# Kernel tuning notes

Measured on AMD Instinct MI355X. Metric: run time of the kernel, lower is better.

The kernel has to match this reference:

```python
import math
import jax, jax.numpy as jnp
import numpy as np

NTYPE, C, H, E = 3, 256, 8, 32  # n_embd=256, n_head=8, edge_dim=32
A1 = 16  # aux_x1 feature dim (aux_x2 dim = E - A1)


def setup_inputs() -> dict:
    key = jax.random.key(0)
    ks = jax.random.split(key, 16)
    B, T1, T2 = 8, 128, 256
    s = 0.02
    return {
        "x1": jax.random.normal(ks[0], (B, T1, C), jnp.float32),
        "x2": jax.random.normal(ks[1], (B, T2, C), jnp.float32),
        "aux_x1": jax.random.normal(ks[2], (B, T1, A1), jnp.float32),
        "aux_x2": jax.random.normal(ks[3], (B, T2, E - A1), jnp.float32),
        "masks": jax.random.randint(ks[4], (NTYPE, B, T1, T2), 0, 2, jnp.int32),
        # per-type linear params, stored (in, out) so y = x @ W + b
        "Wq": jax.random.normal(ks[5], (NTYPE, C, C), jnp.float32) * s,
        "bq": jnp.zeros((NTYPE, C), jnp.float32),
        "Wk": jax.random.normal(ks[6], (NTYPE, C + E, C), jnp.float32) * s,
        "bk": jnp.zeros((NTYPE, C), jnp.float32),
        "Wv": jax.random.normal(ks[7], (NTYPE, C + E, C), jnp.float32) * s,
        "bv": jnp.zeros((NTYPE, C), jnp.float32),
        "Wp": jax.random.normal(ks[8], (NTYPE, C, C), jnp.float32) * s,
        "bp": jnp.zeros((NTYPE, C), jnp.float32),
    }


def _aux_attn(x1, x2, aux_x1, aux_x2, mask, Wq, bq, Wk, bk, Wv, bv, Wp, bp):
    """One AuxCrossAttention type. mask: (B,T1,T2) int."""
    B, T1, _ = x1.shape
    T2 = x2.shape[1]
    hd = C // H
    scale = 1.0 / math.sqrt(hd)

    q = x1 @ Wq + bq  # (B,T1,C)
    # k/v over aug_x2 = [x2 | aux_x1 | aux_x2]; split the linear instead of
    # materializing the (B,T1,T2,C+E) concat (same math by linearity).
    Wk_x, Wk_a1, Wk_a2 = Wk[:C], Wk[C:C + A1], Wk[C + A1:]
    Wv_x, Wv_a1, Wv_a2 = Wv[:C], Wv[C:C + A1], Wv[C + A1:]
    k = (x2 @ Wk_x + aux_x2 @ Wk_a2 + bk)[:, None] + (aux_x1 @ Wk_a1)[:, :, None]  # (B,T1,T2,C)
    v = (x2 @ Wv_x + aux_x2 @ Wv_a2 + bv)[:, None] + (aux_x1 @ Wv_a1)[:, :, None]  # (B,T1,T2,C)

    qh = q.reshape(B, T1, H, hd)
    kh = k.reshape(B, T1, T2, H, hd)
    vh = v.reshape(B, T1, T2, H, hd)

    att = jnp.einsum("bthd,btshd->bhts", qh, kh) * scale  # (B,H,T1,T2)
    valid = (mask != 0)[:, None]  # (B,1,T1,T2)
    att = jnp.where(valid, att, -jnp.inf)
    all_masked = (mask == 0).all(-1)  # (B,T1)
    att = jnp.where(all_masked[:, None, :, None], 0.0, att)
    f = jnp.finfo(att.dtype)
    att = jnp.nan_to_num(att, nan=0.0, posinf=f.max, neginf=f.min)
    att = jax.nn.softmax(att, axis=-1)

    y = jnp.einsum("bhts,btshd->bthd", att, vh).reshape(B, T1, C)
    return y @ Wp + bp


def reference(x1, x2, aux_x1, aux_x2, masks, Wq, bq, Wk, bk, Wv, bv, Wp, bp):
    resid = jnp.zeros_like(x1)
    for i in range(NTYPE):
        resid = resid + _aux_attn(x1, x2, aux_x1, aux_x2, masks[i],
                                  Wq[i], bq[i], Wk[i], bk[i], Wv[i], bv[i], Wp[i], bp[i])
    return resid
```

## Files before the change

kernel.cpp:

```cpp
#include <hip/hip_runtime.h>
#include <hip/hip_bf16.h>

#define NC 256
#define HD 32
#define KE 288

typedef __attribute__((ext_vector_type(8))) short short8;
typedef __attribute__((ext_vector_type(4))) short short4v;
typedef __attribute__((ext_vector_type(4))) float f32x4;

__device__ __forceinline__ unsigned short f2bf(float f) {
    union { float f; unsigned u; } v; v.f = f;
    unsigned r = v.u + 0x7fffu + ((v.u >> 16) & 1u);
    return (unsigned short)(r >> 16);
}

__global__ __launch_bounds__(256) void fused_qkv(
    const float* __restrict__ x1, const float* __restrict__ x2,
    const float* __restrict__ ax1, const float* __restrict__ ax2,
    const float* __restrict__ Wq, const float* __restrict__ bq,
    const float* __restrict__ Wk, const float* __restrict__ bk,
    const float* __restrict__ Wv, const float* __restrict__ bv,
    float* __restrict__ q, float* __restrict__ kb, float* __restrict__ vb,
    float* __restrict__ va)
{
    __shared__ short As[4 * 128 * 8];
    __shared__ short Bs[4 * 128 * 8];

    const int bx = blockIdx.x;
    const float *Aab, *Aaux, *W, *bias;
    float* outp;
    int m0, n0, nfull, auxrow;
    if (bx < 48) {
        const int i = bx >> 4, tile = bx & 15;
        m0 = (tile >> 1) * 128; n0 = (tile & 1) * 128;
        Aab = x1; Aaux = nullptr;
        W = Wq + i * NC * NC; bias = bq + i * NC;
        outp = q + (size_t)i * 1024 * NC; nfull = 8; auxrow = -1;
    } else if (bx < 240) {
        const int idx = bx - 48, i2 = idx >> 5, tile = idx & 31;
        const int i = i2 % 3, kv = i2 / 3;
        m0 = (tile >> 1) * 128; n0 = (tile & 1) * 128;
        Aab = x2; Aaux = ax2;
        W = (kv ? Wv : Wk) + i * KE * NC; bias = (kv ? bv : bk) + i * NC;
        outp = (kv ? vb : kb) + (size_t)i * 2048 * NC; nfull = 8; auxrow = 272;
    } else {
        const int idx = bx - 240, i = idx >> 4, tile = idx & 15;
        m0 = (tile >> 1) * 128; n0 = (tile & 1) * 128;
        Aab = nullptr; Aaux = ax1;
        W = Wv + i * KE * NC; bias = nullptr;
        outp = va + (size_t)i * 1024 * NC; nfull = 0; auxrow = 256;
    }

    const int tid = threadIdx.x;
    const int m8 = tid >> 3, kq = tid & 7;
    const int kk = tid >> 3, nq = tid & 7;
    const int wave = tid >> 6, lane = tid & 63;
    const int wy = wave >> 1, wx = wave & 1;
    const int qd = lane >> 4, ml = lane & 15;

    f32x4 acc[4][4];
#pragma unroll
    for (int a = 0; a < 4; ++a)
#pragma unroll
        for (int b = 0; b < 4; ++b) acc[a][b] = {0.f, 0.f, 0.f, 0.f};

    const int nsteps = nfull + (auxrow >= 0 ? 1 : 0);
    for (int step = 0; step < nsteps; ++step) {
        const bool aux = (step == nfull);
        {
            const float* Ap; int lda, kval;
            if (!aux) { Ap = Aab + (size_t)m0 * NC + step * 32; lda = NC; kval = 32; }
            else      { Ap = Aaux + (size_t)m0 * 16;            lda = 16; kval = 16; }
#pragma unroll
            for (int rep = 0; rep < 4; ++rep) {
                const int m = m8 + rep * 32;
                float4 a4 = {0.f, 0.f, 0.f, 0.f};
                if (kq * 4 < kval) a4 = *(const float4*)(Ap + (size_t)m * lda + kq * 4);
                short4v s;
                s.x = (short)f2bf(a4.x); s.y = (short)f2bf(a4.y);
                s.z = (short)f2bf(a4.z); s.w = (short)f2bf(a4.w);
                *(short4v*)&As[(((kq >> 1) * 128) + m) * 8 + (kq & 1) * 4] = s;
            }
        }
        {
            const int krow0 = aux ? auxrow : step * 32;
            const int kval  = aux ? 16 : 32;
#pragma unroll
            for (int rep = 0; rep < 4; ++rep) {
                const int n = nq * 4 + rep * 32;
                float4 b4 = {0.f, 0.f, 0.f, 0.f};
                if (kk < kval) b4 = *(const float4*)(W + (size_t)(krow0 + kk) * NC + n0 + n);
                const int base = (kk >> 3) * 128;
                const int kw = kk & 7;
                Bs[(base + n + 0) * 8 + kw] = (short)f2bf(b4.x);
                Bs[(base + n + 1) * 8 + kw] = (short)f2bf(b4.y);
                Bs[(base + n + 2) * 8 + kw] = (short)f2bf(b4.z);
                Bs[(base + n + 3) * 8 + kw] = (short)f2bf(b4.w);
            }
        }
        __syncthreads();
        short8 af[4], bfr[4];
#pragma unroll
        for (int mt = 0; mt < 4; ++mt)
            af[mt] = *(const short8*)&As[((qd * 128) + wy * 64 + mt * 16 + ml) * 8];
#pragma unroll
        for (int nt = 0; nt < 4; ++nt)
            bfr[nt] = *(const short8*)&Bs[((qd * 128) + wx * 64 + nt * 16 + ml) * 8];
#pragma unroll
        for (int mt = 0; mt < 4; ++mt)
#pragma unroll
            for (int nt = 0; nt < 4; ++nt)
                acc[mt][nt] = __builtin_amdgcn_mfma_f32_16x16x32_bf16(
                    af[mt], bfr[nt], acc[mt][nt], 0, 0, 0);
        __syncthreads();
    }
#pragma unroll
    for (int nt = 0; nt < 4; ++nt) {
        const int col = n0 + wx * 64 + nt * 16 + ml;
        const float bsv = bias ? bias[col] : 0.f;
#pragma unroll
        for (int mt = 0; mt < 4; ++mt) {
            const int row0 = m0 + wy * 64 + mt * 16 + qd * 4;
#pragma unroll
            for (int r = 0; r < 4; ++r)
                outp[(size_t)(row0 + r) * NC + col] = acc[mt][nt][r] + bsv;
        }
    }
}

__global__ __launch_bounds__(256) void attn_mfma(
    const float* __restrict__ q, const float* __restrict__ kb,
    const float* __restrict__ vb, const float* __restrict__ va,
    const int* __restrict__ masks, float* __restrict__ y)
{
    const int bx = blockIdx.x;
    const int tc = bx & 1, h = (bx >> 1) & 7, b = (bx >> 4) & 7, i = bx >> 7;
    const size_t bb = (size_t)i * 8 + b;

    __shared__ short Ks[4 * 256 * 8];
    __shared__ short Vt[32 * 32 * 8];
    __shared__ short Ps[4][32 * 16 * 8];

    const int tid = threadIdx.x;
    const int wave = tid >> 6, lane = tid & 63;
    const int ml = lane & 15, qd = lane >> 4;

    {
        const float* kp = kb + (bb * 256 + tid) * NC + h * HD;
#pragma unroll
        for (int j = 0; j < 8; ++j) {
            float4 v = *(const float4*)(kp + j * 4);
            short4v s;
            s.x = (short)f2bf(v.x); s.y = (short)f2bf(v.y);
            s.z = (short)f2bf(v.z); s.w = (short)f2bf(v.w);
            *(short4v*)&Ks[(((j >> 1) * 256) + tid) * 8 + (j & 1) * 4] = s;
        }
    }
    {
        const int d = tid & 31, sg8 = tid >> 5;
#pragma unroll
        for (int it = 0; it < 4; ++it) {
            const int s0 = it * 64 + sg8 * 8;
            const float* vp = vb + (bb * 256 + s0) * NC + h * HD + d;
            short8 s8;
#pragma unroll
            for (int u = 0; u < 8; ++u) s8[u] = (short)f2bf(vp[u * NC]);
            *(short8*)&Vt[((s0 >> 3) * 32 + d) * 8] = s8;
        }
    }
    __syncthreads();

    const float qscale = 0.17677669529663687f * 1.4426950408889634f;
    short8 af;
    {
        const int t = tc * 64 + wave * 16 + ml;
        const float* qp = q + (bb * 128 + t) * NC + h * HD + qd * 8;
        float4 q0 = *(const float4*)qp;
        float4 q1 = *(const float4*)(qp + 4);
        af[0] = (short)f2bf(q0.x * qscale); af[1] = (short)f2bf(q0.y * qscale);
        af[2] = (short)f2bf(q0.z * qscale); af[3] = (short)f2bf(q0.w * qscale);
        af[4] = (short)f2bf(q1.x * qscale); af[5] = (short)f2bf(q1.y * qscale);
        af[6] = (short)f2bf(q1.z * qscale); af[7] = (short)f2bf(q1.w * qscale);
    }

    f32x4 sacc[16];
#pragma unroll
    for (int nt = 0; nt < 16; ++nt) sacc[nt] = {0.f, 0.f, 0.f, 0.f};
#pragma unroll
    for (int nt = 0; nt < 16; ++nt) {
        short8 bf = *(const short8*)&Ks[(qd * 256 + nt * 16 + ml) * 8];
        sacc[nt] = __builtin_amdgcn_mfma_f32_16x16x32_bf16(af, bf, sacc[nt], 0, 0, 0);
    }

    const int tb = tc * 64 + wave * 16 + qd * 4;
    const int* mp = masks + bb * 128 * 256 + (size_t)tb * 256 + ml;
    f32x4 rs = {0.f, 0.f, 0.f, 0.f};
#pragma unroll
    for (int nt = 0; nt < 16; ++nt) {
#pragma unroll
        for (int r = 0; r < 4; ++r) {
            const int mk = mp[r * 256 + nt * 16];
            float e = mk ? __builtin_amdgcn_exp2f(sacc[nt][r]) : 0.f;
            sacc[nt][r] = e;
            rs[r] += e;
        }
    }
#pragma unroll
    for (int off = 1; off <= 8; off <<= 1) {
#pragma unroll
        for (int r = 0; r < 4; ++r) rs[r] += __shfl_xor(rs[r], off);
    }
    f32x4 pinv, pfill;
#pragma unroll
    for (int r = 0; r < 4; ++r) {
        const bool z = (rs[r] == 0.f);
        pinv[r]  = z ? 0.f : 1.f / rs[r];
        pfill[r] = z ? (1.f / 256.f) : 0.f;
    }

    short* Pw = &Ps[wave][0];
#pragma unroll
    for (int nt = 0; nt < 16; ++nt) {
        const int sgrp = 2 * nt + (ml >> 3);
        const int pos = ml & 7;
#pragma unroll
        for (int r = 0; r < 4; ++r) {
            const float p = sacc[nt][r] * pinv[r] + pfill[r];
            Pw[(sgrp * 16 + qd * 4 + r) * 8 + pos] = (short)f2bf(p);
        }
    }

    f32x4 oacc[2];
    oacc[0] = {0.f, 0.f, 0.f, 0.f};
    oacc[1] = {0.f, 0.f, 0.f, 0.f};
#pragma unroll
    for (int ks = 0; ks < 8; ++ks) {
        short8 pa = *(const short8*)&Pw[((ks * 4 + qd) * 16 + ml) * 8];
#pragma unroll
        for (int n2 = 0; n2 < 2; ++n2) {
            short8 vf = *(const short8*)&Vt[((ks * 4 + qd) * 32 + n2 * 16 + ml) * 8];
            oacc[n2] = __builtin_amdgcn_mfma_f32_16x16x32_bf16(pa, vf, oacc[n2], 0, 0, 0);
        }
    }

#pragma unroll
    for (int n2 = 0; n2 < 2; ++n2) {
        const int d = n2 * 16 + ml;
#pragma unroll
        for (int r = 0; r < 4; ++r) {
            const size_t idx = (bb * 128 + tb + r) * NC + h * HD + d;
            y[idx] = oacc[n2][r] + va[idx];
        }
    }
}

__global__ __launch_bounds__(256) void proj_mfma(
    const float* __restrict__ y, const float* __restrict__ Wp,
    const float* __restrict__ bp, float* __restrict__ out)
{
    __shared__ short As[4 * 64 * 8];
    __shared__ short Bs[4 * 64 * 8];

    const int bx = blockIdx.x;
    const int m0 = (bx >> 2) * 64, n0 = (bx & 3) * 64;
    const int tid = threadIdx.x;
    const int m8 = tid >> 3, kq = tid & 7;
    const int kk = tid >> 3, nq = tid & 7;
    const int wave = tid >> 6, lane = tid & 63;
    const int wy = wave >> 1, wx = wave & 1;
    const int qd = lane >> 4, ml = lane & 15;

    f32x4 acc[2][2];
#pragma unroll
    for (int a = 0; a < 2; ++a)
#pragma unroll
        for (int b = 0; b < 2; ++b) acc[a][b] = {0.f, 0.f, 0.f, 0.f};

    for (int i = 0; i < 3; ++i) {
        const float* A = y + (size_t)i * 1024 * NC;
        const float* W = Wp + (size_t)i * NC * NC;
        for (int step = 0; step < 8; ++step) {
#pragma unroll
            for (int rep = 0; rep < 2; ++rep) {
                const int m = m8 + rep * 32;
                float4 a4 = *(const float4*)(A + (size_t)(m0 + m) * NC + step * 32 + kq * 4);
                short4v s;
                s.x = (short)f2bf(a4.x); s.y = (short)f2bf(a4.y);
                s.z = (short)f2bf(a4.z); s.w = (short)f2bf(a4.w);
                *(short4v*)&As[(((kq >> 1) * 64) + m) * 8 + (kq & 1) * 4] = s;
            }
#pragma unroll
            for (int rep = 0; rep < 2; ++rep) {
                const int n = nq * 4 + rep * 32;
                float4 b4 = *(const float4*)(W + (size_t)(step * 32 + kk) * NC + n0 + n);
                const int base = (kk >> 3) * 64;
                const int kw = kk & 7;
                Bs[(base + n + 0) * 8 + kw] = (short)f2bf(b4.x);
                Bs[(base + n + 1) * 8 + kw] = (short)f2bf(b4.y);
                Bs[(base + n + 2) * 8 + kw] = (short)f2bf(b4.z);
                Bs[(base + n + 3) * 8 + kw] = (short)f2bf(b4.w);
            }
            __syncthreads();
            short8 af[2], bfr[2];
#pragma unroll
            for (int mt = 0; mt < 2; ++mt)
                af[mt] = *(const short8*)&As[((qd * 64) + wy * 32 + mt * 16 + ml) * 8];
#pragma unroll
            for (int nt = 0; nt < 2; ++nt)
                bfr[nt] = *(const short8*)&Bs[((qd * 64) + wx * 32 + nt * 16 + ml) * 8];
#pragma unroll
            for (int mt = 0; mt < 2; ++mt)
#pragma unroll
                for (int nt = 0; nt < 2; ++nt)
                    acc[mt][nt] = __builtin_amdgcn_mfma_f32_16x16x32_bf16(
                        af[mt], bfr[nt], acc[mt][nt], 0, 0, 0);
            __syncthreads();
        }
    }
#pragma unroll
    for (int nt = 0; nt < 2; ++nt) {
        const int col = n0 + wx * 32 + nt * 16 + ml;
        const float b3 = bp[col] + bp[NC + col] + bp[2 * NC + col];
#pragma unroll
        for (int mt = 0; mt < 2; ++mt) {
            const int row0 = m0 + wy * 32 + mt * 16 + qd * 4;
#pragma unroll
            for (int r = 0; r < 4; ++r)
                out[(size_t)(row0 + r) * NC + col] = acc[mt][nt][r] + b3;
        }
    }
}

extern "C" void kernel_launch(void* const* d_in, const int* in_sizes, int n_in,
                              void* d_out, int out_size, void* d_ws, size_t ws_size,
                              hipStream_t stream)
{
    const float* x1  = (const float*)d_in[0];
    const float* x2  = (const float*)d_in[1];
    const float* ax1 = (const float*)d_in[2];
    const float* ax2 = (const float*)d_in[3];
    const int*   mk  = (const int*)d_in[4];
    const float* Wq  = (const float*)d_in[5];
    const float* bq  = (const float*)d_in[6];
    const float* Wk  = (const float*)d_in[7];
    const float* bk  = (const float*)d_in[8];
    const float* Wv  = (const float*)d_in[9];
    const float* bv  = (const float*)d_in[10];
    const float* Wp  = (const float*)d_in[11];
    const float* bp  = (const float*)d_in[12];

    float* ws = (float*)d_ws;
    float* q  = ws;
    float* kb = q  + 3 * 1024 * 256;
    float* vb = kb + 3 * 2048 * 256;
    float* va = vb + 3 * 2048 * 256;
    float* y  = va + 3 * 1024 * 256;

    fused_qkv<<<dim3(288), 256, 0, stream>>>(x1, x2, ax1, ax2, Wq, bq, Wk, bk,
                                             Wv, bv, q, kb, vb, va);
    attn_mfma<<<dim3(384), 256, 0, stream>>>(q, kb, vb, va, mk, y);
    proj_mfma<<<dim3(64), 256, 0, stream>>>(y, Wp, bp, (float*)d_out);
}
```

Baseline: 135.6 us.

## Pre-convert inputs and weights to bf16 MFMA layouts, pack masks into bitmasks

Adds a prep kernel that converts activations and weights to bf16 in K-contiguous (transposed) layouts and packs the int32 masks into per-row bitmasks. The GEMM and attention kernels then read MFMA fragments straight from global memory with no LDS staging or barriers. Intermediates q, k, transposed v and y are stored in bf16, which halves their traffic. This costs an extra kernel launch and a weight conversion on every call, and the fragment loads from global memory may be less coalesced than the old staged path.

```diff
diff --git a/kernel.cpp b/kernel.cpp
--- a/kernel.cpp
+++ b/kernel.cpp
@@ -3,7 +3,6 @@
 
 #define NC 256
 #define HD 32
-#define KE 288
 
 typedef __attribute__((ext_vector_type(8))) short short8;
 typedef __attribute__((ext_vector_type(4))) short short4v;
@@ -14,47 +13,157 @@
     unsigned r = v.u + 0x7fffu + ((v.u >> 16) & 1u);
     return (unsigned short)(r >> 16);
 }
-
-__global__ __launch_bounds__(256) void fused_qkv(
+__device__ __forceinline__ short8 cvt8(float4 a, float4 b) {
+    short8 s;
+    s[0] = (short)f2bf(a.x); s[1] = (short)f2bf(a.y);
+    s[2] = (short)f2bf(a.z); s[3] = (short)f2bf(a.w);
+    s[4] = (short)f2bf(b.x); s[5] = (short)f2bf(b.y);
+    s[6] = (short)f2bf(b.z); s[7] = (short)f2bf(b.w);
+    return s;
+}
+
+__global__ __launch_bounds__(256) void prep(
     const float* __restrict__ x1, const float* __restrict__ x2,
     const float* __restrict__ ax1, const float* __restrict__ ax2,
-    const float* __restrict__ Wq, const float* __restrict__ bq,
-    const float* __restrict__ Wk, const float* __restrict__ bk,
-    const float* __restrict__ Wv, const float* __restrict__ bv,
-    float* __restrict__ q, float* __restrict__ kb, float* __restrict__ vb,
-    float* __restrict__ va)
+    const float* __restrict__ Wq, const float* __restrict__ Wk,
+    const float* __restrict__ Wv, const float* __restrict__ Wp,
+    const int* __restrict__ masks,
+    short* __restrict__ x1b, short* __restrict__ A2, short* __restrict__ ax1p,
+    short* __restrict__ WqT, short* __restrict__ WkT, short* __restrict__ WvT,
+    short* __restrict__ WvA1T, short* __restrict__ WpT,
+    unsigned int* __restrict__ mb)
 {
-    __shared__ short As[4 * 128 * 8];
-    __shared__ short Bs[4 * 128 * 8];
-
+    const int bx = blockIdx.x, tid = threadIdx.x;
+    const short8 zero8 = {0, 0, 0, 0, 0, 0, 0, 0};
+
+    if (bx < 64) {
+        const size_t base = ((size_t)bx * 256 + tid) * 16;
+        const float* p = x1 + base;
+        float4 a = *(const float4*)p,       b = *(const float4*)(p + 4);
+        float4 c = *(const float4*)(p + 8), d = *(const float4*)(p + 12);
+        *(short8*)&x1b[base]     = cvt8(a, b);
+        *(short8*)&x1b[base + 8] = cvt8(c, d);
+    } else if (bx < 96) {
+        const int r0 = (bx - 64) * 64;
+        for (int rr = 0; rr < 64; ++rr) {
+            const int row = r0 + rr;
+            A2[row * 288 + tid] = (short)f2bf(x2[(size_t)row * 256 + tid]);
+            if (tid < 16)
+                A2[row * 288 + 256 + tid] = (short)f2bf(ax2[row * 16 + tid]);
+            else if (tid < 32)
+                A2[row * 288 + 256 + tid] = 0;
+        }
+    } else if (bx < 100) {
+        const int row = (bx - 96) * 256 + tid;
+        const float* p = ax1 + (size_t)row * 16;
+        float4 a = *(const float4*)p,       b = *(const float4*)(p + 4);
+        float4 c = *(const float4*)(p + 8), d = *(const float4*)(p + 12);
+        short* o = ax1p + (size_t)row * 32;
+        *(short8*)o        = cvt8(a, b);
+        *(short8*)(o + 8)  = cvt8(c, d);
+        *(short8*)(o + 16) = zero8;
+        *(short8*)(o + 24) = zero8;
+    } else if (bx < 112) {
+        const int idx = bx - 100, i = idx >> 2, o0 = (idx & 3) * 8;
+        const float* W = Wq + (size_t)i * 256 * 256;
+        short* O = WqT + (size_t)i * 256 * 256;
+        for (int o = o0; o < o0 + 8; ++o) {
+            short8 s;
+#pragma unroll
+            for (int j = 0; j < 8; ++j) s[j] = (short)f2bf(W[(size_t)(o * 8 + j) * 256 + tid]);
+            *(short8*)&O[(size_t)tid * 256 + o * 8] = s;
+        }
+    } else if (bx < 136) {
+        const int idx = bx - 112, kv = idx / 12, sub = idx % 12;
+        const int i = sub >> 2, o0 = (sub & 3) * 9;
+        const float* W = (kv ? Wv : Wk) + (size_t)i * 288 * 256;
+        short* O = (kv ? WvT : WkT) + (size_t)i * 256 * 288;
+        for (int o = o0; o < o0 + 9; ++o) {
+            short8 s;
+#pragma unroll
+            for (int j = 0; j < 8; ++j) {
+                const int kp = o * 8 + j;
+                const int src = (kp < 256) ? kp : (kp < 272 ? kp + 16 : -1);
+                s[j] = (src >= 0) ? (short)f2bf(W[(size_t)src * 256 + tid]) : (short)0;
+            }
+            *(short8*)&O[(size_t)tid * 288 + o * 8] = s;
+        }
+    } else if (bx < 139) {
+        const int i = bx - 136;
+        const float* W = Wv + (size_t)i * 288 * 256;
+        short* O = WvA1T + (size_t)i * 256 * 32;
+        short8 s0, s1;
+#pragma unroll
+        for (int j = 0; j < 8; ++j) {
+            s0[j] = (short)f2bf(W[(size_t)(256 + j) * 256 + tid]);
+            s1[j] = (short)f2bf(W[(size_t)(264 + j) * 256 + tid]);
+        }
+        short* o = O + (size_t)tid * 32;
+        *(short8*)o = s0; *(short8*)(o + 8) = s1;
+        *(short8*)(o + 16) = zero8; *(short8*)(o + 24) = zero8;
+    } else if (bx < 151) {
+        const int idx = bx - 139, i = idx >> 2, o0 = (idx & 3) * 8;
+        const float* W = Wp + (size_t)i * 256 * 256;
+        short* O = WpT + (size_t)i * 256 * 256;
+        for (int o = o0; o < o0 + 8; ++o) {
+            short8 s;
+#pragma unroll
+            for (int j = 0; j < 8; ++j) s[j] = (short)f2bf(W[(size_t)(o * 8 + j) * 256 + tid]);
+            *(short8*)&O[(size_t)tid * 256 + o * 8] = s;
+        }
+    } else {
+        const int r0 = (bx - 151) * 64;
+        const int wave = tid >> 6, lane = tid & 63;
+        for (int rr = 0; rr < 64; ++rr) {
+            const int row = r0 + rr;
+            const int mk = masks[(size_t)row * 256 + tid];
+            unsigned long long bal = __ballot(mk != 0);
+            if (lane == 0) {
+                mb[row * 8 + wave * 2 + 0] = (unsigned int)bal;
+                mb[row * 8 + wave * 2 + 1] = (unsigned int)(bal >> 32);
+            }
+        }
+    }
+}
+
+__global__ __launch_bounds__(256) void fused_gemm(
+    const short* __restrict__ x1b, const short* __restrict__ A2,
+    const short* __restrict__ ax1p,
+    const short* __restrict__ WqT, const short* __restrict__ WkT,
+    const short* __restrict__ WvT, const short* __restrict__ WvA1T,
+    const float* __restrict__ bq, const float* __restrict__ bk,
+    const float* __restrict__ bv,
+    short* __restrict__ qb, short* __restrict__ kbb,
+    short* __restrict__ vbT, float* __restrict__ va)
+{
     const int bx = blockIdx.x;
-    const float *Aab, *Aaux, *W, *bias;
-    float* outp;
-    int m0, n0, nfull, auxrow;
+    const short *Ab, *Wb;
+    const float* bias = nullptr;
+    short* outb = nullptr; float* outf = nullptr;
+    int LDA, LDW, nsteps, mode, m0, n0;
     if (bx < 48) {
-        const int i = bx >> 4, tile = bx & 15;
-        m0 = (tile >> 1) * 128; n0 = (tile & 1) * 128;
-        Aab = x1; Aaux = nullptr;
-        W = Wq + i * NC * NC; bias = bq + i * NC;
-        outp = q + (size_t)i * 1024 * NC; nfull = 8; auxrow = -1;
+        const int i = bx >> 4, t = bx & 15;
+        m0 = (t >> 1) * 128; n0 = (t & 1) * 128;
+        Ab = x1b; LDA = 256; Wb = WqT + (size_t)i * 256 * 256; LDW = 256;
+        nsteps = 8; bias = bq + i * 256; outb = qb + (size_t)i * 1024 * 256; mode = 0;
+    } else if (bx < 144) {
+        const int idx = bx - 48, i = idx >> 5, t = idx & 31;
+        m0 = (t >> 1) * 128; n0 = (t & 1) * 128;
+        Ab = A2; LDA = 288; Wb = WkT + (size_t)i * 256 * 288; LDW = 288;
+        nsteps = 9; bias = bk + i * 256; outb = kbb + (size_t)i * 2048 * 256; mode = 0;
     } else if (bx < 240) {
-        const int idx = bx - 48, i2 = idx >> 5, tile = idx & 31;
-        const int i = i2 % 3, kv = i2 / 3;
-        m0 = (tile >> 1) * 128; n0 = (tile & 1) * 128;
-        Aab = x2; Aaux = ax2;
-        W = (kv ? Wv : Wk) + i * KE * NC; bias = (kv ? bv : bk) + i * NC;
-        outp = (kv ? vb : kb) + (size_t)i * 2048 * NC; nfull = 8; auxrow = 272;
+        const int idx = bx - 144, i = idx >> 5, t = idx & 31;
+        m0 = (t >> 1) * 128; n0 = (t & 1) * 128;
+        Ab = A2; LDA = 288; Wb = WvT + (size_t)i * 256 * 288; LDW = 288;
+        nsteps = 9; bias = bv + i * 256; outb = vbT + (size_t)i * 256 * 2048; mode = 1;
     } else {
-        const int idx = bx - 240, i = idx >> 4, tile = idx & 15;
-        m0 = (tile >> 1) * 128; n0 = (tile & 1) * 128;
-        Aab = nullptr; Aaux = ax1;
-        W = Wv + i * KE * NC; bias = nullptr;
-        outp = va + (size_t)i * 1024 * NC; nfull = 0; auxrow = 256;
+        const int idx = bx - 240, i = idx >> 4, t = idx & 15;
+        m0 = (t >> 1) * 128; n0 = (t & 1) * 128;
+        Ab = ax1p; LDA = 32; Wb = WvA1T + (size_t)i * 256 * 32; LDW = 32;
+        nsteps = 1; outf = va + (size_t)i * 1024 * 256; mode = 2;
     }
 
     const int tid = threadIdx.x;
-    const int m8 = tid >> 3, kq = tid & 7;
-    const int kk = tid >> 3, nq = tid & 7;
     const int wave = tid >> 6, lane = tid & 63;
     const int wy = wave >> 1, wx = wave & 1;
     const int qd = lane >> 4, ml = lane & 15;
@@ -65,56 +174,22 @@
 #pragma unroll
         for (int b = 0; b < 4; ++b) acc[a][b] = {0.f, 0.f, 0.f, 0.f};
 
-    const int nsteps = nfull + (auxrow >= 0 ? 1 : 0);
     for (int step = 0; step < nsteps; ++step) {
-        const bool aux = (step == nfull);
-        {
-            const float* Ap; int lda, kval;
-            if (!aux) { Ap = Aab + (size_t)m0 * NC + step * 32; lda = NC; kval = 32; }
-            else      { Ap = Aaux + (size_t)m0 * 16;            lda = 16; kval = 16; }
-#pragma unroll
-            for (int rep = 0; rep < 4; ++rep) {
-                const int m = m8 + rep * 32;
-                float4 a4 = {0.f, 0.f, 0.f, 0.f};
-                if (kq * 4 < kval) a4 = *(const float4*)(Ap + (size_t)m * lda + kq * 4);
-                short4v s;
-                s.x = (short)f2bf(a4.x); s.y = (short)f2bf(a4.y);
-                s.z = (short)f2bf(a4.z); s.w = (short)f2bf(a4.w);
-                *(short4v*)&As[(((kq >> 1) * 128) + m) * 8 + (kq & 1) * 4] = s;
-            }
-        }
-        {
-            const int krow0 = aux ? auxrow : step * 32;
-            const int kval  = aux ? 16 : 32;
-#pragma unroll
-            for (int rep = 0; rep < 4; ++rep) {
-                const int n = nq * 4 + rep * 32;
-                float4 b4 = {0.f, 0.f, 0.f, 0.f};
-                if (kk < kval) b4 = *(const float4*)(W + (size_t)(krow0 + kk) * NC + n0 + n);
-                const int base = (kk >> 3) * 128;
-                const int kw = kk & 7;
-                Bs[(base + n + 0) * 8 + kw] = (short)f2bf(b4.x);
-                Bs[(base + n + 1) * 8 + kw] = (short)f2bf(b4.y);
-                Bs[(base + n + 2) * 8 + kw] = (short)f2bf(b4.z);
-                Bs[(base + n + 3) * 8 + kw] = (short)f2bf(b4.w);
-            }
-        }
-        __syncthreads();
-        short8 af[4], bfr[4];
+        short8 af[4], bf[4];
 #pragma unroll
         for (int mt = 0; mt < 4; ++mt)
-            af[mt] = *(const short8*)&As[((qd * 128) + wy * 64 + mt * 16 + ml) * 8];
+            af[mt] = *(const short8*)&Ab[(size_t)(m0 + wy * 64 + mt * 16 + ml) * LDA + step * 32 + qd * 8];
 #pragma unroll
         for (int nt = 0; nt < 4; ++nt)
-            bfr[nt] = *(const short8*)&Bs[((qd * 128) + wx * 64 + nt * 16 + ml) * 8];
+            bf[nt] = *(const short8*)&Wb[(size_t)(n0 + wx * 64 + nt * 16 + ml) * LDW + step * 32 + qd * 8];
 #pragma unroll
         for (int mt = 0; mt < 4; ++mt)
 #pragma unroll
             for (int nt = 0; nt < 4; ++nt)
                 acc[mt][nt] = __builtin_amdgcn_mfma_f32_16x16x32_bf16(
-                    af[mt], bfr[nt], acc[mt][nt], 0, 0, 0);
-        __syncthreads();
-    }
+                    af[mt], bf[nt], acc[mt][nt], 0, 0, 0);
+    }
+
 #pragma unroll
     for (int nt = 0; nt < 4; ++nt) {
         const int col = n0 + wx * 64 + nt * 16 + ml;
@@ -122,66 +197,52 @@
 #pragma unroll
         for (int mt = 0; mt < 4; ++mt) {
             const int row0 = m0 + wy * 64 + mt * 16 + qd * 4;
-#pragma unroll
-            for (int r = 0; r < 4; ++r)
-                outp[(size_t)(row0 + r) * NC + col] = acc[mt][nt][r] + bsv;
+            if (mode == 0) {
+#pragma unroll
+                for (int r = 0; r < 4; ++r)
+                    outb[(size_t)(row0 + r) * 256 + col] = (short)f2bf(acc[mt][nt][r] + bsv);
+            } else if (mode == 1) {
+                short4v s;
+                s.x = (short)f2bf(acc[mt][nt][0] + bsv);
+                s.y = (short)f2bf(acc[mt][nt][1] + bsv);
+                s.z = (short)f2bf(acc[mt][nt][2] + bsv);
+                s.w = (short)f2bf(acc[mt][nt][3] + bsv);
+                *(short4v*)&outb[(size_t)col * 2048 + row0] = s;
+            } else {
+#pragma unroll
+                for (int r = 0; r < 4; ++r)
+                    outf[(size_t)(row0 + r) * 256 + col] = acc[mt][nt][r];
+            }
         }
     }
 }
 
 __global__ __launch_bounds__(256) void attn_mfma(
-    const float* __restrict__ q, const float* __restrict__ kb,
-    const float* __restrict__ vb, const float* __restrict__ va,
-    const int* __restrict__ masks, float* __restrict__ y)
+    const short* __restrict__ qb, const short* __restrict__ kbb,
+    const short* __restrict__ vbT, const float* __restrict__ va,
+    const unsigned int* __restrict__ mb, short* __restrict__ yb)
 {
     const int bx = blockIdx.x;
     const int tc = bx & 1, h = (bx >> 1) & 7, b = (bx >> 4) & 7, i = bx >> 7;
     const size_t bb = (size_t)i * 8 + b;
 
-    __shared__ short Ks[4 * 256 * 8];
-    __shared__ short Vt[32 * 32 * 8];
     __shared__ short Ps[4][32 * 16 * 8];
 
     const int tid = threadIdx.x;
     const int wave = tid >> 6, lane = tid & 63;
     const int ml = lane & 15, qd = lane >> 4;
-
-    {
-        const float* kp = kb + (bb * 256 + tid) * NC + h * HD;
-#pragma unroll
-        for (int j = 0; j < 8; ++j) {
-            float4 v = *(const float4*)(kp + j * 4);
-            short4v s;
-            s.x = (short)f2bf(v.x); s.y = (short)f2bf(v.y);
-            s.z = (short)f2bf(v.z); s.w = (short)f2bf(v.w);
-            *(short4v*)&Ks[(((j >> 1) * 256) + tid) * 8 + (j & 1) * 4] = s;
-        }
-    }
-    {
-        const int d = tid & 31, sg8 = tid >> 5;
-#pragma unroll
-        for (int it = 0; it < 4; ++it) {
-            const int s0 = it * 64 + sg8 * 8;
-            const float* vp = vb + (bb * 256 + s0) * NC + h * HD + d;
-            short8 s8;
-#pragma unroll
-            for (int u = 0; u < 8; ++u) s8[u] = (short)f2bf(vp[u * NC]);
-            *(short8*)&Vt[((s0 >> 3) * 32 + d) * 8] = s8;
-        }
-    }
-    __syncthreads();
 
     const float qscale = 0.17677669529663687f * 1.4426950408889634f;
     short8 af;
     {
         const int t = tc * 64 + wave * 16 + ml;
-        const float* qp = q + (bb * 128 + t) * NC + h * HD + qd * 8;
-        float4 q0 = *(const float4*)qp;
-        float4 q1 = *(const float4*)(qp + 4);
-        af[0] = (short)f2bf(q0.x * qscale); af[1] = (short)f2bf(q0.y * qscale);
-        af[2] = (short)f2bf(q0.z * qscale); af[3] = (short)f2bf(q0.w * qscale);
-        af[4] = (short)f2bf(q1.x * qscale); af[5] = (short)f2bf(q1.y * qscale);
-        af[6] = (short)f2bf(q1.z * qscale); af[7] = (short)f2bf(q1.w * qscale);
+        short8 qr = *(const short8*)&qb[(bb * 128 + t) * 256 + h * HD + qd * 8];
+#pragma unroll
+        for (int j = 0; j < 8; ++j) {
+            union { float f; unsigned u; } v;
+            v.u = ((unsigned)(unsigned short)qr[j]) << 16;
+            af[j] = (short)f2bf(v.f * qscale);
+        }
     }
 
     f32x4 sacc[16];
@@ -189,18 +250,32 @@
     for (int nt = 0; nt < 16; ++nt) sacc[nt] = {0.f, 0.f, 0.f, 0.f};
 #pragma unroll
     for (int nt = 0; nt < 16; ++nt) {
-        short8 bf = *(const short8*)&Ks[(qd * 256 + nt * 16 + ml) * 8];
+        short8 bf = *(const short8*)&kbb[(bb * 256 + nt * 16 + ml) * 256 + h * HD + qd * 8];
         sacc[nt] = __builtin_amdgcn_mfma_f32_16x16x32_bf16(af, bf, sacc[nt], 0, 0, 0);
     }
 
     const int tb = tc * 64 + wave * 16 + qd * 4;
-    const int* mp = masks + bb * 128 * 256 + (size_t)tb * 256 + ml;
+    uint4 wlo[4], whi[4];
+#pragma unroll
+    for (int r = 0; r < 4; ++r) {
+        const unsigned int* p = mb + (bb * 128 + tb + r) * 8;
+        wlo[r] = *(const uint4*)p;
+        whi[r] = *(const uint4*)(p + 4);
+    }
+
     f32x4 rs = {0.f, 0.f, 0.f, 0.f};
 #pragma unroll
     for (int nt = 0; nt < 16; ++nt) {
 #pragma unroll
         for (int r = 0; r < 4; ++r) {
-            const int mk = mp[r * 256 + nt * 16];
+            unsigned int w;
+            switch (nt >> 1) {
+                case 0: w = wlo[r].x; break; case 1: w = wlo[r].y; break;
+                case 2: w = wlo[r].z; break; case 3: w = wlo[r].w; break;
+                case 4: w = whi[r].x; break; case 5: w = whi[r].y; break;
+                case 6: w = whi[r].z; break; default: w = whi[r].w; break;
+            }
+            const bool mk = (w >> ((nt & 1) * 16 + ml)) & 1u;
             float e = mk ? __builtin_amdgcn_exp2f(sacc[nt][r]) : 0.f;
             sacc[nt][r] = e;
             rs[r] += e;
@@ -234,39 +309,35 @@
     f32x4 oacc[2];
     oacc[0] = {0.f, 0.f, 0.f, 0.f};
     oacc[1] = {0.f, 0.f, 0.f, 0.f};
+    const short* Vb = vbT + (size_t)i * 256 * 2048 + (size_t)b * 256;
 #pragma unroll
     for (int ks = 0; ks < 8; ++ks) {
         short8 pa = *(const short8*)&Pw[((ks * 4 + qd) * 16 + ml) * 8];
 #pragma unroll
         for (int n2 = 0; n2 < 2; ++n2) {
-            short8 vf = *(const short8*)&Vt[((ks * 4 + qd) * 32 + n2 * 16 + ml) * 8];
+            short8 vf = *(const short8*)&Vb[(size_t)(h * HD + n2 * 16 + ml) * 2048 + ks * 32 + qd * 8];
             oacc[n2] = __builtin_amdgcn_mfma_f32_16x16x32_bf16(pa, vf, oacc[n2], 0, 0, 0);
         }
     }
 
 #pragma unroll
     for (int n2 = 0; n2 < 2; ++n2) {
-        const int d = n2 * 16 + ml;
+        const int d = h * HD + n2 * 16 + ml;
 #pragma unroll
         for (int r = 0; r < 4; ++r) {
-            const size_t idx = (bb * 128 + tb + r) * NC + h * HD + d;
-            y[idx] = oacc[n2][r] + va[idx];
-        }
-    }
-}
-
-__global__ __launch_bounds__(256) void proj_mfma(
-    const float* __restrict__ y, const float* __restrict__ Wp,
+            const size_t idx = (bb * 128 + tb + r) * 256 + d;
+            yb[idx] = (short)f2bf(oacc[n2][r] + va[idx]);
+        }
+    }
+}
+
+__global__ __launch_bounds__(256) void proj2(
+    const short* __restrict__ yb, const short* __restrict__ WpT,
     const float* __restrict__ bp, float* __restrict__ out)
 {
-    __shared__ short As[4 * 64 * 8];
-    __shared__ short Bs[4 * 64 * 8];
-
     const int bx = blockIdx.x;
     const int m0 = (bx >> 2) * 64, n0 = (bx & 3) * 64;
     const int tid = threadIdx.x;
-    const int m8 = tid >> 3, kq = tid & 7;
-    const int kk = tid >> 3, nq = tid & 7;
     const int wave = tid >> 6, lane = tid & 63;
     const int wy = wave >> 1, wx = wave & 1;
     const int qd = lane >> 4, ml = lane & 15;
@@ -278,56 +349,35 @@
         for (int b = 0; b < 2; ++b) acc[a][b] = {0.f, 0.f, 0.f, 0.f};
 
     for (int i = 0; i < 3; ++i) {
-        const float* A = y + (size_t)i * 1024 * NC;
-        const float* W = Wp + (size_t)i * NC * NC;
+        const short* A = yb + (size_t)i * 1024 * 256;
+        const short* W = WpT + (size_t)i * 256 * 256;
+#pragma unroll
         for (int step = 0; step < 8; ++step) {
-#pragma unroll
-            for (int rep = 0; rep < 2; ++rep) {
-                const int m = m8 + rep * 32;
-                float4 a4 = *(const float4*)(A + (size_t)(m0 + m) * NC + step * 32 + kq * 4);
-                short4v s;
-                s.x = (short)f2bf(a4.x); s.y = (short)f2bf(a4.y);
-                s.z = (short)f2bf(a4.z); s.w = (short)f2bf(a4.w);
-                *(short4v*)&As[(((kq >> 1) * 64) + m) * 8 + (kq & 1) * 4] = s;
-            }
-#pragma unroll
-            for (int rep = 0; rep < 2; ++rep) {
-                const int n = nq * 4 + rep * 32;
-                float4 b4 = *(const float4*)(W + (size_t)(step * 32 + kk) * NC + n0 + n);
-                const int base = (kk >> 3) * 64;
-                const int kw = kk & 7;
-                Bs[(base + n + 0) * 8 + kw] = (short)f2bf(b4.x);
-                Bs[(base + n + 1) * 8 + kw] = (short)f2bf(b4.y);
-                Bs[(base + n + 2) * 8 + kw] = (short)f2bf(b4.z);
-                Bs[(base + n + 3) * 8 + kw] = (short)f2bf(b4.w);
-            }
-            __syncthreads();
-            short8 af[2], bfr[2];
+            short8 af[2], bf[2];
 #pragma unroll
             for (int mt = 0; mt < 2; ++mt)
-                af[mt] = *(const short8*)&As[((qd * 64) + wy * 32 + mt * 16 + ml) * 8];
+                af[mt] = *(const short8*)&A[(size_t)(m0 + wy * 32 + mt * 16 + ml) * 256 + step * 32 + qd * 8];
 #pragma unroll
             for (int nt = 0; nt < 2; ++nt)
-                bfr[nt] = *(const short8*)&Bs[((qd * 64) + wx * 32 + nt * 16 + ml) * 8];
+                bf[nt] = *(const short8*)&W[(size_t)(n0 + wx * 32 + nt * 16 + ml) * 256 + step * 32 + qd * 8];
 #pragma unroll
             for (int mt = 0; mt < 2; ++mt)
 #pragma unroll
                 for (int nt = 0; nt < 2; ++nt)
                     acc[mt][nt] = __builtin_amdgcn_mfma_f32_16x16x32_bf16(
-                        af[mt], bfr[nt], acc[mt][nt], 0, 0, 0);
-            __syncthreads();
+                        af[mt], bf[nt], acc[mt][nt], 0, 0, 0);
         }
     }
 #pragma unroll
     for (int nt = 0; nt < 2; ++nt) {
         const int col = n0 + wx * 32 + nt * 16 + ml;
-        const float b3 = bp[col] + bp[NC + col] + bp[2 * NC + col];
+        const float b3 = bp[col] + bp[256 + col] + bp[512 + col];
 #pragma unroll
         for (int mt = 0; mt < 2; ++mt) {
             const int row0 = m0 + wy * 32 + mt * 16 + qd * 4;
 #pragma unroll
             for (int r = 0; r < 4; ++r)
-                out[(size_t)(row0 + r) * NC + col] = acc[mt][nt][r] + b3;
+                out[(size_t)(row0 + r) * 256 + col] = acc[mt][nt][r] + b3;
         }
     }
 }
@@ -350,15 +400,27 @@
     const float* Wp  = (const float*)d_in[11];
     const float* bp  = (const float*)d_in[12];
 
-    float* ws = (float*)d_ws;
-    float* q  = ws;
-    float* kb = q  + 3 * 1024 * 256;
-    float* vb = kb + 3 * 2048 * 256;
-    float* va = vb + 3 * 2048 * 256;
-    float* y  = va + 3 * 1024 * 256;
-
-    fused_qkv<<<dim3(288), 256, 0, stream>>>(x1, x2, ax1, ax2, Wq, bq, Wk, bk,
-                                             Wv, bv, q, kb, vb, va);
-    attn_mfma<<<dim3(384), 256, 0, stream>>>(q, kb, vb, va, mk, y);
-    proj_mfma<<<dim3(64), 256, 0, stream>>>(y, Wp, bp, (float*)d_out);
-}
+    char* w = (char*)d_ws;
+    short* x1b   = (short*)(w + 0);
+    short* A2    = (short*)(w + 524288);
+    short* ax1p  = (short*)(w + 1703936);
+    short* WqT   = (short*)(w + 1769472);
+    short* WkT   = (short*)(w + 2162688);
+    short* WvT   = (short*)(w + 2605056);
+    short* WvA1T = (short*)(w + 3047424);
+    short* WpT   = (short*)(w + 3096576);
+    unsigned int* mbits = (unsigned int*)(w + 3489792);
+    short* qb    = (short*)(w + 3588096);
+    short* kbb   = (short*)(w + 5160960);
+    short* vbT   = (short*)(w + 8306688);
+    float* va    = (float*)(w + 11452416);
+    short* yb    = (short*)(w + 14598144);
+
+    prep<<<dim3(199), 256, 0, stream>>>(x1, x2, ax1, ax2, Wq, Wk, Wv, Wp, mk,
+                                        x1b, A2, ax1p, WqT, WkT, WvT, WvA1T,
+                                        WpT, mbits);
+    fused_gemm<<<dim3(288), 256, 0, stream>>>(x1b, A2, ax1p, WqT, WkT, WvT,
+                                              WvA1T, bq, bk, bv, qb, kbb, vbT, va);
+    attn_mfma<<<dim3(384), 256, 0, stream>>>(qb, kbb, vbT, va, mbits, yb);
+    proj2<<<dim3(64), 256, 0, stream>>>(yb, WpT, bp, (float*)d_out);
+}
```

Result: slower. 153.1 us (+13.0%).
